# Optimization experiments

Measured on AMD Instinct MI355X. Metric: run time of the kernel, lower is better.

Reference implementation:

```python
import jax, jax.numpy as jnp
import numpy as np

# ---- DMP constants (from DMPParameters with N=5, tau=1, dt=1/(T*l), Dof=9, a_z=25) ----
N_BASIS = 5
T_STEPS = 10
L_SUB = 10
DIM = 9                      # len(state_index)
TAU = 1.0
DT = TAU / (T_STEPS * L_SUB)            # 0.01
TIME_STEPS = int(round(TAU / DT)) + 1   # 101
A_X = 1.0
A_Z = 25.0
B_Z = A_Z / 4.0
_c_np = np.exp(-A_X * np.linspace(0.0, 1.0, N_BASIS))
C = jnp.asarray(_c_np, dtype=jnp.float32)                          # rbf centers
H = jnp.asarray(N_BASIS ** 1.5 / _c_np / A_X, dtype=jnp.float32)   # rbf widths (sigma2)


def _integrate(w, y0, dy0, goal):
    """Euler integration of the DMP dynamical system.
    w: (R, N) basis weights; y0, dy0, goal: (R,) with R = batch*DIM.
    Returns Y: (R, TIME_STEPS) positions."""
    scale = goal - y0  # fixed forcing-term scaling

    def step(carry, _):
        y, z, x = carry
        x = x + (-A_X * x / TAU) * DT                  # canonical system
        psi = jnp.exp(-H * (x - C) ** 2)               # (N,) gaussian rbf
        fx = (w @ psi) * x * scale / jnp.sum(psi)      # (R,) forcing term
        dz = (A_Z * (B_Z * (goal - y) - z) + fx) / TAU
        dy = z / TAU
        y = y + dy * DT
        z = z + dz * DT
        return (y, z, x), y

    z0 = dy0 * TAU
    _, ys = jax.lax.scan(step, (y0, z0, jnp.float32(1.0)), None, length=TIME_STEPS - 1)
    # prepend initial position, transpose to (R, TIME_STEPS)
    return jnp.concatenate([y0[None, :], ys], axis=0).T


def setup_inputs():
    key = jax.random.key(0)
    ks = jax.random.split(key, 4)
    B, D_IN, HID = 16384, 128, 2048
    out_size = DIM * (N_BASIS + 1)  # 54 = N*dim + dim
    return {
        "input": jax.random.normal(ks[0], (B, D_IN), jnp.float32),
        "W0": jax.random.normal(ks[1], (HID, D_IN), jnp.float32) / np.sqrt(D_IN),
        "b0": jnp.full((HID,), 0.1, jnp.float32),
        "W1": jax.random.normal(ks[2], (HID, HID), jnp.float32) / np.sqrt(HID),
        "b1": jnp.full((HID,), 0.1, jnp.float32),
        "Wl": jax.random.normal(ks[3], (out_size, HID), jnp.float32) / np.sqrt(HID),
        "bl": jnp.zeros((out_size,), jnp.float32),
    }


def reference(input, W0, b0, W1, b1, Wl, bl):
    B = input.shape[0]
    # MLP backbone with tanh hidden activation
    h = jnp.tanh(input @ W0.T + b0)
    h = jnp.tanh(h @ W1.T + b1)
    out = (h @ Wl.T + bl) * 100.0                          # (B, DIM*(N+1))
    # split DMP parameters: goal then basis weights
    goal = out[:, :DIM].reshape(-1)                        # (B*DIM,)
    w = out[:, DIM:DIM * (N_BASIS + 1)].reshape(-1, N_BASIS)  # (B*DIM, N)
    y0 = input[:, 7:16].reshape(-1)                        # state_index
    dy0 = input[:, 22:31].reshape(-1)                      # vel_index
    Y = _integrate(w, y0, dy0, goal)                       # (B*DIM, 101)
    y = Y.reshape(B, DIM, TIME_STEPS)[:, :, ::L_SUB]       # (B, DIM, T+1)
    return y[:, :, 1:] - y[:, :, :-1]                      # (B, DIM, T)
```

## Files before the change

kernel.cpp:

```cpp
#include <hip/hip_runtime.h>
#include <hip/hip_fp16.h>
#include <math.h>

typedef _Float16 f16;
typedef _Float16 f16x8 __attribute__((ext_vector_type(8)));
typedef _Float16 f16x4v __attribute__((ext_vector_type(4)));
typedef float f32x4 __attribute__((ext_vector_type(4)));

#define B_SZ 16384
#define D_INP 128
#define HID 2048
#define DIMS 9
#define OUTC 54
#define OUTP 64
#define NZ3 4

__device__ __forceinline__ void load_lds16(const f16* g, f16* l) {
    __builtin_amdgcn_global_load_lds(
        (__attribute__((address_space(1))) void*)(g),
        (__attribute__((address_space(3))) void*)(l),
        16, 0, 0);
}

__device__ __forceinline__ float fast_tanh(float x) {
    float e = __builtin_amdgcn_exp2f(2.885390081777927f * x);
    return 1.0f - 2.0f * __builtin_amdgcn_rcpf(e + 1.0f);
}

#define N4_W0  (HID * D_INP / 4)
#define N4_W1  (HID * HID / 4)
#define N4_WL  (OUTP * HID / 4)
__global__ __launch_bounds__(256) void cvt_fused_kernel(
    const float* __restrict__ W0, const float* __restrict__ W1,
    const float* __restrict__ Wl,
    f16* __restrict__ w0q, f16* __restrict__ w1q, f16* __restrict__ wlq)
{
    int i = blockIdx.x * 256 + threadIdx.x;
    const float* s; f16* d; int j;
    if (i < N4_W0) { s = W0; d = w0q; j = i; }
    else if (i < N4_W0 + N4_W1) { s = W1; d = w1q; j = i - N4_W0; }
    else {
        j = i - N4_W0 - N4_W1;
        int e0 = j * 4, row = e0 >> 11, col = e0 & (HID - 1);
        f16x4v o;
        if (row < OUTC) {
            float4 v = ((const float4*)Wl)[(row * HID + col) >> 2];
            o.x = (f16)v.x; o.y = (f16)v.y; o.z = (f16)v.z; o.w = (f16)v.w;
        } else {
            o.x = (f16)0.f; o.y = (f16)0.f; o.z = (f16)0.f; o.w = (f16)0.f;
        }
        ((f16x4v*)wlq)[j] = o;
        return;
    }
    float4 v = ((const float4*)s)[j];
    f16x4v o;
    o.x = (f16)v.x; o.y = (f16)v.y; o.z = (f16)v.z; o.w = (f16)v.w;
    ((f16x4v*)d)[j] = o;
}

template <int BN, int EPI>
__global__ __launch_bounds__(256, 2) void gemm_nt(
    const f16* __restrict__ A, const f16* __restrict__ Bm,
    const float* __restrict__ bias, void* __restrict__ Cout,
    int M, int N, int K, int bias_n)
{
    constexpr int BM = 128, BK = 64;
    constexpr int NI = BN / 32;
    __shared__ __align__(16) f16 sa[BM * BK];
    __shared__ __align__(16) f16 sb[BN * BK];

    const int tid  = threadIdx.x;
    const int lane = tid & 63;
    const int wave = tid >> 6;
    const int wm = wave >> 1, wn = wave & 1;

    const int flat = blockIdx.x + blockIdx.y * gridDim.x;
    const int gsz  = 8 * gridDim.y;
    const int grp  = flat / gsz;
    const int rem  = flat - grp * gsz;
    const int m0 = (grp * 8 + (rem & 7)) * BM;
    const int n0 = (rem >> 3) * BN;

    const int k_len = K / gridDim.z;
    const int k_beg = blockIdx.z * k_len;
    const int k_end = k_beg + k_len;

    f32x4 acc[4][NI];
    #pragma unroll
    for (int i = 0; i < 4; ++i)
        #pragma unroll
        for (int j = 0; j < NI; ++j) acc[i][j] = (f32x4){0.f, 0.f, 0.f, 0.f};

    const int r8 = lane >> 3;
    const int cg = (((lane & 7) ^ r8) << 3);

    for (int k0 = k_beg; k0 < k_end; k0 += BK) {
        #pragma unroll
        for (int c = 0; c < (BM * BK * 2) / 4096; ++c) {
            int o = c * 4096 + wave * 1024;
            const f16* gp = A + (size_t)(m0 + (o >> 7) + r8) * K + k0 + cg;
            load_lds16(gp, (f16*)((char*)sa + o));
        }
        #pragma unroll
        for (int c = 0; c < (BN * BK * 2) / 4096; ++c) {
            int o = c * 4096 + wave * 1024;
            const f16* gp = Bm + (size_t)(n0 + (o >> 7) + r8) * K + k0 + cg;
            load_lds16(gp, (f16*)((char*)sb + o));
        }
        __syncthreads();

        #pragma unroll
        for (int kc = 0; kc < 2; ++kc) {
            f16x8 af[4], bf[NI];
            #pragma unroll
            for (int mi = 0; mi < 4; ++mi) {
                int ar = wm * 64 + mi * 16 + (lane & 15);
                af[mi] = *(const f16x8*)&sa[ar * 64 + ((((kc << 2) | (lane >> 4)) ^ (ar & 7)) << 3)];
            }
            #pragma unroll
            for (int ni = 0; ni < NI; ++ni) {
                int br = wn * (BN / 2) + ni * 16 + (lane & 15);
                bf[ni] = *(const f16x8*)&sb[br * 64 + ((((kc << 2) | (lane >> 4)) ^ (br & 7)) << 3)];
            }
            #pragma unroll
            for (int mi = 0; mi < 4; ++mi)
                #pragma unroll
                for (int ni = 0; ni < NI; ++ni)
                    acc[mi][ni] = __builtin_amdgcn_mfma_f32_16x16x32_f16(af[mi], bf[ni], acc[mi][ni], 0, 0, 0);
        }
        __syncthreads();
    }

    const int crow0 = m0 + wm * 64 + (lane >> 4) * 4;
    const int ccol0 = n0 + wn * (BN / 2) + (lane & 15);
    if (EPI == 0) {
        f16* C = (f16*)Cout;
        #pragma unroll
        for (int mi = 0; mi < 4; ++mi)
            #pragma unroll
            for (int ni = 0; ni < NI; ++ni) {
                int col = ccol0 + ni * 16;
                float bv = bias[col];
                #pragma unroll
                for (int r2 = 0; r2 < 4; ++r2) {
                    float v = fast_tanh(acc[mi][ni][r2] + bv);
                    C[(size_t)(crow0 + mi * 16 + r2) * N + col] = (f16)v;
                }
            }
    } else {
        float* C = (float*)Cout + (size_t)blockIdx.z * M * N;
        #pragma unroll
        for (int mi = 0; mi < 4; ++mi)
            #pragma unroll
            for (int ni = 0; ni < NI; ++ni) {
                int col = ccol0 + ni * 16;
                float bv = (blockIdx.z == 0 && col < bias_n) ? bias[col] * 100.0f : 0.0f;
                #pragma unroll
                for (int r2 = 0; r2 < 4; ++r2) {
                    float v = acc[mi][ni][r2] * 100.0f + bv;
                    C[(size_t)(crow0 + mi * 16 + r2) * N + col] = v;
                }
            }
    }
}

__global__ __launch_bounds__(256, 2) void gemm1_f32a(
    const float* __restrict__ A, const f16* __restrict__ Bm,
    const float* __restrict__ bias, f16* __restrict__ C)
{
    constexpr int BM = 128, BK = 64, BN = 128, NI = 4;
    constexpr int N = HID, K = D_INP;
    __shared__ __align__(16) f16 sa[BM * BK];
    __shared__ __align__(16) f16 sb[BN * BK];

    const int tid  = threadIdx.x;
    const int lane = tid & 63;
    const int wave = tid >> 6;
    const int wm = wave >> 1, wn = wave & 1;

    const int flat = blockIdx.x + blockIdx.y * gridDim.x;
    const int gsz  = 8 * gridDim.y;
    const int grp  = flat / gsz;
    const int rem  = flat - grp * gsz;
    const int m0 = (grp * 8 + (rem & 7)) * BM;
    const int n0 = (rem >> 3) * BN;

    f32x4 acc[4][NI];
    #pragma unroll
    for (int i = 0; i < 4; ++i)
        #pragma unroll
        for (int j = 0; j < NI; ++j) acc[i][j] = (f32x4){0.f, 0.f, 0.f, 0.f};

    const int r8 = lane >> 3;
    const int cg = (((lane & 7) ^ r8) << 3);

    for (int k0 = 0; k0 < K; k0 += BK) {
        #pragma unroll
        for (int c = 0; c < (BM * BK * 2) / 4096; ++c) {
            int o = c * 4096 + wave * 1024;
            const float* gp = A + (size_t)(m0 + (o >> 7) + r8) * K + k0 + cg;
            float4 v0 = *(const float4*)gp;
            float4 v1 = *(const float4*)(gp + 4);
            f16x8 h;
            h[0] = (f16)v0.x; h[1] = (f16)v0.y; h[2] = (f16)v0.z; h[3] = (f16)v0.w;
            h[4] = (f16)v1.x; h[5] = (f16)v1.y; h[6] = (f16)v1.z; h[7] = (f16)v1.w;
            *(f16x8*)((char*)sa + o + (lane << 4)) = h;
        }
        #pragma unroll
        for (int c = 0; c < (BN * BK * 2) / 4096; ++c) {
            int o = c * 4096 + wave * 1024;
            const f16* gp = Bm + (size_t)(n0 + (o >> 7) + r8) * K + k0 + cg;
            load_lds16(gp, (f16*)((char*)sb + o));
        }
        __syncthreads();

        #pragma unroll
        for (int kc = 0; kc < 2; ++kc) {
            f16x8 af[4], bf[NI];
            #pragma unroll
            for (int mi = 0; mi < 4; ++mi) {
                int ar = wm * 64 + mi * 16 + (lane & 15);
                af[mi] = *(const f16x8*)&sa[ar * 64 + ((((kc << 2) | (lane >> 4)) ^ (ar & 7)) << 3)];
            }
            #pragma unroll
            for (int ni = 0; ni < NI; ++ni) {
                int br = wn * 64 + ni * 16 + (lane & 15);
                bf[ni] = *(const f16x8*)&sb[br * 64 + ((((kc << 2) | (lane >> 4)) ^ (br & 7)) << 3)];
            }
            #pragma unroll
            for (int mi = 0; mi < 4; ++mi)
                #pragma unroll
                for (int ni = 0; ni < NI; ++ni)
                    acc[mi][ni] = __builtin_amdgcn_mfma_f32_16x16x32_f16(af[mi], bf[ni], acc[mi][ni], 0, 0, 0);
        }
        __syncthreads();
    }

    const int crow0 = m0 + wm * 64 + (lane >> 4) * 4;
    const int ccol0 = n0 + wn * 64 + (lane & 15);
    #pragma unroll
    for (int mi = 0; mi < 4; ++mi)
        #pragma unroll
        for (int ni = 0; ni < NI; ++ni) {
            int col = ccol0 + ni * 16;
            float bv = bias[col];
            #pragma unroll
            for (int r2 = 0; r2 < 4; ++r2) {
                float v = fast_tanh(acc[mi][ni][r2] + bv);
                C[(size_t)(crow0 + mi * 16 + r2) * N + col] = (f16)v;
            }
        }
}

__global__ __launch_bounds__(256) void integrate_kernel(
    const float* __restrict__ out3p, const float* __restrict__ input,
    float* __restrict__ out)
{
    __shared__ float g[500];
    {
        int k = threadIdx.x;
        if (k < 100) {
            float x = expf(-0.010050335853501441f * (float)(k + 1));
            float psi[5], ssum = 0.0f;
            #pragma unroll
            for (int n = 0; n < 5; ++n) {
                float c = expf(-0.25f * (float)n);
                float h = 11.180339887498949f / c;
                float dx = x - c;
                psi[n] = expf(-h * dx * dx);
                ssum += psi[n];
            }
            float inv = x / ssum;
            #pragma unroll
            for (int n = 0; n < 5; ++n) g[k * 5 + n] = psi[n] * inv;
        }
    }
    __syncthreads();

    int r = blockIdx.x * 256 + threadIdx.x;
    int b = r / DIMS, d = r - b * DIMS;

    float goal = 0.f, w0 = 0.f, w1 = 0.f, w2 = 0.f, w3 = 0.f, w4 = 0.f;
    #pragma unroll
    for (int z = 0; z < NZ3; ++z) {
        const float* ob = out3p + (size_t)z * B_SZ * OUTP + (size_t)b * OUTP;
        goal += ob[d];
        w0 += ob[DIMS + d * 5 + 0];
        w1 += ob[DIMS + d * 5 + 1];
        w2 += ob[DIMS + d * 5 + 2];
        w3 += ob[DIMS + d * 5 + 3];
        w4 += ob[DIMS + d * 5 + 4];
    }

    float y = input[(size_t)b * D_INP + 7 + d];
    float z = input[(size_t)b * D_INP + 22 + d];
    const float scale = goal - y;

    float prev = y;
    float* op = out + (size_t)b * (DIMS * 10) + d * 10;
    int j = 0;
    for (int k = 0; k < 100; ++k) {
        const float* gk = &g[k * 5];
        float fx = scale * (w0 * gk[0] + w1 * gk[1] + w2 * gk[2] + w3 * gk[3] + w4 * gk[4]);
        float dz = 25.0f * (6.25f * (goal - y) - z) + fx;
        y = y + z * 0.01f;
        z = z + dz * 0.01f;
        if ((k % 10) == 9) { op[j] = y - prev; prev = y; ++j; }
    }
}

extern "C" void kernel_launch(void* const* d_in, const int* in_sizes, int n_in,
                              void* d_out, int out_size, void* d_ws, size_t ws_size,
                              hipStream_t stream) {
    (void)in_sizes; (void)n_in; (void)out_size; (void)ws_size;
    const float* input = (const float*)d_in[0];
    const float* W0 = (const float*)d_in[1];
    const float* b0 = (const float*)d_in[2];
    const float* W1 = (const float*)d_in[3];
    const float* b1 = (const float*)d_in[4];
    const float* Wl = (const float*)d_in[5];
    const float* bl = (const float*)d_in[6];
    float* out = (float*)d_out;

    f16* w0q = (f16*)d_ws;
    f16* w1q = w0q + (size_t)HID * D_INP;
    f16* wlq = w1q + (size_t)HID * HID;
    f16* h1  = wlq + (size_t)OUTP * HID;
    f16* h2  = h1 + (size_t)B_SZ * HID;
    float* out3p = (float*)h1;

    int n4_total = N4_W0 + N4_W1 + N4_WL;
    cvt_fused_kernel<<<(n4_total + 255) / 256, 256, 0, stream>>>(
        W0, W1, Wl, w0q, w1q, wlq);

    gemm1_f32a<<<dim3(B_SZ / 128, HID / 128), 256, 0, stream>>>(
        input, w0q, b0, h1);
    gemm_nt<128, 0><<<dim3(B_SZ / 128, HID / 128, 1), 256, 0, stream>>>(
        h1, w1q, b1, (void*)h2, B_SZ, HID, HID, HID);
    gemm_nt<64, 1><<<dim3(B_SZ / 128, 1, NZ3), 256, 0, stream>>>(
        h2, wlq, bl, (void*)out3p, B_SZ, OUTP, HID, OUTC);

    integrate_kernel<<<B_SZ * DIMS / 256, 256, 0, stream>>>(out3p, input, out);
}
```

Baseline: 256.8 us.

## Fuse weight fp16 conversion into first GEMM and load full K tile

```diff
diff --git a/kernel.cpp b/kernel.cpp
--- a/kernel.cpp
+++ b/kernel.cpp
@@ -25,37 +25,6 @@
 __device__ __forceinline__ float fast_tanh(float x) {
     float e = __builtin_amdgcn_exp2f(2.885390081777927f * x);
     return 1.0f - 2.0f * __builtin_amdgcn_rcpf(e + 1.0f);
-}
-
-#define N4_W0  (HID * D_INP / 4)
-#define N4_W1  (HID * HID / 4)
-#define N4_WL  (OUTP * HID / 4)
-__global__ __launch_bounds__(256) void cvt_fused_kernel(
-    const float* __restrict__ W0, const float* __restrict__ W1,
-    const float* __restrict__ Wl,
-    f16* __restrict__ w0q, f16* __restrict__ w1q, f16* __restrict__ wlq)
-{
-    int i = blockIdx.x * 256 + threadIdx.x;
-    const float* s; f16* d; int j;
-    if (i < N4_W0) { s = W0; d = w0q; j = i; }
-    else if (i < N4_W0 + N4_W1) { s = W1; d = w1q; j = i - N4_W0; }
-    else {
-        j = i - N4_W0 - N4_W1;
-        int e0 = j * 4, row = e0 >> 11, col = e0 & (HID - 1);
-        f16x4v o;
-        if (row < OUTC) {
-            float4 v = ((const float4*)Wl)[(row * HID + col) >> 2];
-            o.x = (f16)v.x; o.y = (f16)v.y; o.z = (f16)v.z; o.w = (f16)v.w;
-        } else {
-            o.x = (f16)0.f; o.y = (f16)0.f; o.z = (f16)0.f; o.w = (f16)0.f;
-        }
-        ((f16x4v*)wlq)[j] = o;
-        return;
-    }
-    float4 v = ((const float4*)s)[j];
-    f16x4v o;
-    o.x = (f16)v.x; o.y = (f16)v.y; o.z = (f16)v.z; o.w = (f16)v.w;
-    ((f16x4v*)d)[j] = o;
 }
 
 template <int BN, int EPI>
@@ -164,26 +133,48 @@
     }
 }
 
-__global__ __launch_bounds__(256, 2) void gemm1_f32a(
-    const float* __restrict__ A, const f16* __restrict__ Bm,
-    const float* __restrict__ bias, f16* __restrict__ C)
+__global__ __launch_bounds__(256, 2) void gemm1_fused(
+    const float* __restrict__ A, const float* __restrict__ W0,
+    const float* __restrict__ bias,
+    const float* __restrict__ W1, const float* __restrict__ Wl,
+    f16* __restrict__ w1q, f16* __restrict__ wlq,
+    f16* __restrict__ C)
 {
-    constexpr int BM = 128, BK = 64, BN = 128, NI = 4;
+    constexpr int NI = 4;
     constexpr int N = HID, K = D_INP;
-    __shared__ __align__(16) f16 sa[BM * BK];
-    __shared__ __align__(16) f16 sb[BN * BK];
+    __shared__ __align__(16) f16 sa[128 * 128];
+    __shared__ __align__(16) f16 sb[128 * 128];
 
     const int tid  = threadIdx.x;
     const int lane = tid & 63;
     const int wave = tid >> 6;
     const int wm = wave >> 1, wn = wave & 1;
-
-    const int flat = blockIdx.x + blockIdx.y * gridDim.x;
-    const int gsz  = 8 * gridDim.y;
-    const int grp  = flat / gsz;
-    const int rem  = flat - grp * gsz;
-    const int m0 = (grp * 8 + (rem & 7)) * BM;
-    const int n0 = (rem >> 3) * BN;
+    const int m0 = blockIdx.x * 128;
+    const int n0 = blockIdx.y * 128;
+    const int bid = blockIdx.x + blockIdx.y * gridDim.x;
+
+    {
+        int i0 = bid * 512 + tid;
+        #pragma unroll
+        for (int j = 0; j < 2; ++j) {
+            int idx = i0 + j * 256;
+            float4 v = ((const float4*)W1)[idx];
+            f16x4v o; o.x = (f16)v.x; o.y = (f16)v.y; o.z = (f16)v.z; o.w = (f16)v.w;
+            ((f16x4v*)w1q)[idx] = o;
+        }
+        if (bid < 128) {
+            int idx = bid * 256 + tid;
+            int row = (idx * 4) >> 11;
+            f16x4v o;
+            if (row < OUTC) {
+                float4 v = ((const float4*)Wl)[idx];
+                o.x = (f16)v.x; o.y = (f16)v.y; o.z = (f16)v.z; o.w = (f16)v.w;
+            } else {
+                o.x = (f16)0.f; o.y = (f16)0.f; o.z = (f16)0.f; o.w = (f16)0.f;
+            }
+            ((f16x4v*)wlq)[idx] = o;
+        }
+    }
 
     f32x4 acc[4][NI];
     #pragma unroll
@@ -191,14 +182,13 @@
         #pragma unroll
         for (int j = 0; j < NI; ++j) acc[i][j] = (f32x4){0.f, 0.f, 0.f, 0.f};
 
-    const int r8 = lane >> 3;
-    const int cg = (((lane & 7) ^ r8) << 3);
-
-    for (int k0 = 0; k0 < K; k0 += BK) {
-        #pragma unroll
-        for (int c = 0; c < (BM * BK * 2) / 4096; ++c) {
-            int o = c * 4096 + wave * 1024;
-            const float* gp = A + (size_t)(m0 + (o >> 7) + r8) * K + k0 + cg;
+    #pragma unroll
+    for (int c = 0; c < 8; ++c) {
+        int o = c * 4096 + wave * 1024;
+        int row = (o >> 8) + (lane >> 4);
+        int gch = (lane & 15) ^ (row & 15);
+        {
+            const float* gp = A + (size_t)(m0 + row) * K + gch * 8;
             float4 v0 = *(const float4*)gp;
             float4 v1 = *(const float4*)(gp + 4);
             f16x8 h;
@@ -206,34 +196,37 @@
             h[4] = (f16)v1.x; h[5] = (f16)v1.y; h[6] = (f16)v1.z; h[7] = (f16)v1.w;
             *(f16x8*)((char*)sa + o + (lane << 4)) = h;
         }
-        #pragma unroll
-        for (int c = 0; c < (BN * BK * 2) / 4096; ++c) {
-            int o = c * 4096 + wave * 1024;
-            const f16* gp = Bm + (size_t)(n0 + (o >> 7) + r8) * K + k0 + cg;
-            load_lds16(gp, (f16*)((char*)sb + o));
-        }
-        __syncthreads();
-
-        #pragma unroll
-        for (int kc = 0; kc < 2; ++kc) {
-            f16x8 af[4], bf[NI];
-            #pragma unroll
-            for (int mi = 0; mi < 4; ++mi) {
-                int ar = wm * 64 + mi * 16 + (lane & 15);
-                af[mi] = *(const f16x8*)&sa[ar * 64 + ((((kc << 2) | (lane >> 4)) ^ (ar & 7)) << 3)];
-            }
-            #pragma unroll
-            for (int ni = 0; ni < NI; ++ni) {
-                int br = wn * 64 + ni * 16 + (lane & 15);
-                bf[ni] = *(const f16x8*)&sb[br * 64 + ((((kc << 2) | (lane >> 4)) ^ (br & 7)) << 3)];
-            }
-            #pragma unroll
-            for (int mi = 0; mi < 4; ++mi)
-                #pragma unroll
-                for (int ni = 0; ni < NI; ++ni)
-                    acc[mi][ni] = __builtin_amdgcn_mfma_f32_16x16x32_f16(af[mi], bf[ni], acc[mi][ni], 0, 0, 0);
-        }
-        __syncthreads();
+        {
+            const float* gp = W0 + (size_t)(n0 + row) * K + gch * 8;
+            float4 v0 = *(const float4*)gp;
+            float4 v1 = *(const float4*)(gp + 4);
+            f16x8 h;
+            h[0] = (f16)v0.x; h[1] = (f16)v0.y; h[2] = (f16)v0.z; h[3] = (f16)v0.w;
+            h[4] = (f16)v1.x; h[5] = (f16)v1.y; h[6] = (f16)v1.z; h[7] = (f16)v1.w;
+            *(f16x8*)((char*)sb + o + (lane << 4)) = h;
+        }
+    }
+    __syncthreads();
+
+    #pragma unroll
+    for (int kc = 0; kc < 4; ++kc) {
+        const int ch = (kc << 2) | (lane >> 4);
+        f16x8 af[4], bf[NI];
+        #pragma unroll
+        for (int mi = 0; mi < 4; ++mi) {
+            int ar = wm * 64 + mi * 16 + (lane & 15);
+            af[mi] = *(const f16x8*)&sa[ar * 128 + ((ch ^ (ar & 15)) << 3)];
+        }
+        #pragma unroll
+        for (int ni = 0; ni < NI; ++ni) {
+            int br = wn * 64 + ni * 16 + (lane & 15);
+            bf[ni] = *(const f16x8*)&sb[br * 128 + ((ch ^ (br & 15)) << 3)];
+        }
+        #pragma unroll
+        for (int mi = 0; mi < 4; ++mi)
+            #pragma unroll
+            for (int ni = 0; ni < NI; ++ni)
+                acc[mi][ni] = __builtin_amdgcn_mfma_f32_16x16x32_f16(af[mi], bf[ni], acc[mi][ni], 0, 0, 0);
     }
 
     const int crow0 = m0 + wm * 64 + (lane >> 4) * 4;
@@ -322,19 +315,14 @@
     const float* bl = (const float*)d_in[6];
     float* out = (float*)d_out;
 
-    f16* w0q = (f16*)d_ws;
-    f16* w1q = w0q + (size_t)HID * D_INP;
+    f16* w1q = (f16*)d_ws;
     f16* wlq = w1q + (size_t)HID * HID;
     f16* h1  = wlq + (size_t)OUTP * HID;
     f16* h2  = h1 + (size_t)B_SZ * HID;
     float* out3p = (float*)h1;
 
-    int n4_total = N4_W0 + N4_W1 + N4_WL;
-    cvt_fused_kernel<<<(n4_total + 255) / 256, 256, 0, stream>>>(
-        W0, W1, Wl, w0q, w1q, wlq);
-
-    gemm1_f32a<<<dim3(B_SZ / 128, HID / 128), 256, 0, stream>>>(
-        input, w0q, b0, h1);
+    gemm1_fused<<<dim3(B_SZ / 128, HID / 128), 256, 0, stream>>>(
+        input, W0, b0, W1, Wl, w1q, wlq, h1);
     gemm_nt<128, 0><<<dim3(B_SZ / 128, HID / 128, 1), 256, 0, stream>>>(
         h1, w1q, b1, (void*)h2, B_SZ, HID, HID, HID);
     gemm_nt<64, 1><<<dim3(B_SZ / 128, 1, NZ3), 256, 0, stream>>>(
```

After: 286.2 us. 11.5% more time.

## Pre-pack W1 into MFMA fragment layout and load B directly to registers

Applied to the files above, without the earlier changes.

```diff
diff --git a/kernel.cpp b/kernel.cpp
--- a/kernel.cpp
+++ b/kernel.cpp
@@ -33,29 +33,35 @@
 __global__ __launch_bounds__(256) void cvt_fused_kernel(
     const float* __restrict__ W0, const float* __restrict__ W1,
     const float* __restrict__ Wl,
-    f16* __restrict__ w0q, f16* __restrict__ w1q, f16* __restrict__ wlq)
+    f16* __restrict__ w0q, f16* __restrict__ w1p, f16* __restrict__ wlq)
 {
     int i = blockIdx.x * 256 + threadIdx.x;
-    const float* s; f16* d; int j;
-    if (i < N4_W0) { s = W0; d = w0q; j = i; }
-    else if (i < N4_W0 + N4_W1) { s = W1; d = w1q; j = i - N4_W0; }
-    else {
-        j = i - N4_W0 - N4_W1;
-        int e0 = j * 4, row = e0 >> 11, col = e0 & (HID - 1);
+    if (i < N4_W0) {
+        float4 v = ((const float4*)W0)[i];
+        f16x4v o; o.x = (f16)v.x; o.y = (f16)v.y; o.z = (f16)v.z; o.w = (f16)v.w;
+        ((f16x4v*)w0q)[i] = o;
+    } else if (i < N4_W0 + N4_W1) {
+        int j = i - N4_W0;
+        int n = j >> 9;
+        int k = (j & 511) << 2;
+        float4 v = ((const float4*)W1)[j];
+        f16x4v o; o.x = (f16)v.x; o.y = (f16)v.y; o.z = (f16)v.z; o.w = (f16)v.w;
+        int blk   = ((n >> 4) << 6) | (k >> 5);
+        int lanep = (((k >> 3) & 3) << 4) | (n & 15);
+        int off   = (blk << 9) + (lanep << 3) + (k & 7);
+        *(f16x4v*)(w1p + off) = o;
+    } else {
+        int j = i - N4_W0 - N4_W1;
+        int e0 = j * 4, row = e0 >> 11;
         f16x4v o;
         if (row < OUTC) {
-            float4 v = ((const float4*)Wl)[(row * HID + col) >> 2];
+            float4 v = ((const float4*)Wl)[j];
             o.x = (f16)v.x; o.y = (f16)v.y; o.z = (f16)v.z; o.w = (f16)v.w;
         } else {
             o.x = (f16)0.f; o.y = (f16)0.f; o.z = (f16)0.f; o.w = (f16)0.f;
         }
         ((f16x4v*)wlq)[j] = o;
-        return;
-    }
-    float4 v = ((const float4*)s)[j];
-    f16x4v o;
-    o.x = (f16)v.x; o.y = (f16)v.y; o.z = (f16)v.z; o.w = (f16)v.w;
-    ((f16x4v*)d)[j] = o;
+    }
 }
 
 template <int BN, int EPI>
@@ -162,6 +168,86 @@
                 }
             }
     }
+}
+
+__global__ __launch_bounds__(256, 2) void gemm2_bpacked(
+    const f16* __restrict__ A, const f16* __restrict__ Bp,
+    const float* __restrict__ bias, f16* __restrict__ C)
+{
+    constexpr int BM = 128, BK = 64, NI = 4;
+    constexpr int N = HID, K = HID;
+    __shared__ __align__(16) f16 sa[BM * BK];
+
+    const int tid  = threadIdx.x;
+    const int lane = tid & 63;
+    const int wave = tid >> 6;
+    const int wm = wave >> 1, wn = wave & 1;
+
+    const int flat = blockIdx.x + blockIdx.y * gridDim.x;
+    const int gsz  = 8 * gridDim.y;
+    const int grp  = flat / gsz;
+    const int rem  = flat - grp * gsz;
+    const int m0 = (grp * 8 + (rem & 7)) * BM;
+    const int n0 = (rem >> 3) * 128;
+
+    f32x4 acc[4][NI];
+    #pragma unroll
+    for (int i = 0; i < 4; ++i)
+        #pragma unroll
+        for (int j = 0; j < NI; ++j) acc[i][j] = (f32x4){0.f, 0.f, 0.f, 0.f};
+
+    const int r8 = lane >> 3;
+    const int cg = (((lane & 7) ^ r8) << 3);
+
+    const f16* bbase = Bp + (((size_t)(n0 >> 4) + wn * 4) << 15) + (lane << 3);
+
+    for (int k0 = 0; k0 < K; k0 += BK) {
+        #pragma unroll
+        for (int c = 0; c < 4; ++c) {
+            int o = c * 4096 + wave * 1024;
+            const f16* gp = A + (size_t)(m0 + (o >> 7) + r8) * K + k0 + cg;
+            load_lds16(gp, (f16*)((char*)sa + o));
+        }
+        f16x8 bf[2][NI];
+        const int kb = k0 >> 5;
+        #pragma unroll
+        for (int kc = 0; kc < 2; ++kc)
+            #pragma unroll
+            for (int ni = 0; ni < NI; ++ni)
+                bf[kc][ni] = *(const f16x8*)(bbase + (((ni << 6) + kb + kc) << 9));
+        __syncthreads();
+
+        #pragma unroll
+        for (int kc = 0; kc < 2; ++kc) {
+            f16x8 af[4];
+            #pragma unroll
+            for (int mi = 0; mi < 4; ++mi) {
+                int ar = wm * 64 + mi * 16 + (lane & 15);
+                af[mi] = *(const f16x8*)&sa[ar * 64 + ((((kc << 2) | (lane >> 4)) ^ (ar & 7)) << 3)];
+            }
+            #pragma unroll
+            for (int mi = 0; mi < 4; ++mi)
+                #pragma unroll
+                for (int ni = 0; ni < NI; ++ni)
+                    acc[mi][ni] = __builtin_amdgcn_mfma_f32_16x16x32_f16(af[mi], bf[kc][ni], acc[mi][ni], 0, 0, 0);
+        }
+        __syncthreads();
+    }
+
+    const int crow0 = m0 + wm * 64 + (lane >> 4) * 4;
+    const int ccol0 = n0 + wn * 64 + (lane & 15);
+    #pragma unroll
+    for (int mi = 0; mi < 4; ++mi)
+        #pragma unroll
+        for (int ni = 0; ni < NI; ++ni) {
+            int col = ccol0 + ni * 16;
+            float bv = bias[col];
+            #pragma unroll
+            for (int r2 = 0; r2 < 4; ++r2) {
+                float v = fast_tanh(acc[mi][ni][r2] + bv);
+                C[(size_t)(crow0 + mi * 16 + r2) * N + col] = (f16)v;
+            }
+        }
 }
 
 __global__ __launch_bounds__(256, 2) void gemm1_f32a(
@@ -323,20 +409,20 @@
     float* out = (float*)d_out;
 
     f16* w0q = (f16*)d_ws;
-    f16* w1q = w0q + (size_t)HID * D_INP;
-    f16* wlq = w1q + (size_t)HID * HID;
+    f16* w1p = w0q + (size_t)HID * D_INP;
+    f16* wlq = w1p + (size_t)HID * HID;
     f16* h1  = wlq + (size_t)OUTP * HID;
     f16* h2  = h1 + (size_t)B_SZ * HID;
     float* out3p = (float*)h1;
 
     int n4_total = N4_W0 + N4_W1 + N4_WL;
     cvt_fused_kernel<<<(n4_total + 255) / 256, 256, 0, stream>>>(
-        W0, W1, Wl, w0q, w1q, wlq);
+        W0, W1, Wl, w0q, w1p, wlq);
 
     gemm1_f32a<<<dim3(B_SZ / 128, HID / 128), 256, 0, stream>>>(
         input, w0q, b0, h1);
-    gemm_nt<128, 0><<<dim3(B_SZ / 128, HID / 128, 1), 256, 0, stream>>>(
-        h1, w1q, b1, (void*)h2, B_SZ, HID, HID, HID);
+    gemm2_bpacked<<<dim3(B_SZ / 128, HID / 128), 256, 0, stream>>>(
+        h1, w1p, b1, h2);
     gemm_nt<64, 1><<<dim3(B_SZ / 128, 1, NZ3), 256, 0, stream>>>(
         h2, wlq, bl, (void*)out3p, B_SZ, OUTP, HID, OUTC);
 
```

New measurement: 273.2 us. 1.06x slower.
